# Optimization experiments

Hardware: AMD Instinct MI355X
Metric: run time of the kernel (lower is better)

## Reference

```python
import jax, jax.numpy as jnp
import numpy as np

T1 = 0.2
T2 = 1.2
LABEL_SMOOTHING = 0.05
NUM_ITERS = 20  # fixed-point iterations for lambda_t_a (t2 > 1 branch)


def log_t(x, t):
    # tempered log (t != 1)
    return (x ** (1.0 - t) - 1.0) / (1.0 - t)


def exp_t(x, t):
    # tempered exp (t != 1): relu((1-t)x + 1) ** (1/(1-t))
    return jnp.maximum((1.0 - t) * x + 1.0, 0.0) ** (1.0 / (1.0 - t))


def lambda_t_a(a, t):
    # t > 1 fixed-point branch of the original torch code, with a fixed
    # iteration count instead of a host-synced convergence check.
    mu = jnp.max(a, axis=-1, keepdims=True)            # [N, 1]
    norm_a_initial = a - mu                            # [N, C], <= 0

    def body(norm_a, _):
        z_a = jnp.sum(exp_t(norm_a, t), axis=-1, keepdims=True)  # [N, 1]
        return z_a ** (1.0 - t) * norm_a_initial, None

    norm_a, _ = jax.lax.scan(body, norm_a_initial, None, length=NUM_ITERS)
    z_a = jnp.sum(exp_t(norm_a, t), axis=-1, keepdims=True)
    return -log_t(1.0 / z_a, t) + mu                   # [N, 1]


def setup_inputs() -> dict:
    key = jax.random.key(0)
    k1, k2 = jax.random.split(key)
    N, C = 16384, 1000
    inputs = jax.random.normal(k1, (N, C), dtype=jnp.float32)
    labels = jax.random.randint(k2, (N,), 0, C)
    targets = jax.nn.one_hot(labels, C, dtype=jnp.float32)
    return {"inputs": inputs, "targets": targets}


def reference(inputs, targets):
    num_classes = targets.shape[-1]
    # label smoothing (label_smoothing > 0 branch)
    targets = (1.0 - num_classes / (num_classes - 1) * LABEL_SMOOTHING) * targets \
              + LABEL_SMOOTHING / (num_classes - 1)
    norm_constants = lambda_t_a(inputs, T2)                      # [N, 1]
    probabilities = exp_t(inputs - norm_constants, T2)           # [N, C]
    loss1 = targets * (log_t(targets + 1e-8, T1) - log_t(probabilities, T1))
    loss2 = (targets ** (2.0 - T1) - probabilities ** (2.0 - T1)) / (2.0 - T1)
    out = jnp.sum(loss1 - loss2, axis=-1)                        # [N]
    return jnp.mean(out)
```

## Files before the change

kernel.cpp:

```cpp
#include <hip/hip_runtime.h>
#include <math.h>

#define C_DIM 1000
#define BIG   1.0e30f

__device__ __forceinline__ float fexp2(float x) { return __builtin_amdgcn_exp2f(x); }
__device__ __forceinline__ float flog2(float x) { return __builtin_amdgcn_logf(x); }
__device__ __forceinline__ float frcp(float x)  { return __builtin_amdgcn_rcpf(x); }

template <int CTRL, int RM>
__device__ __forceinline__ float dpp_add_term(float x) {
    int y = __builtin_amdgcn_update_dpp(0, __float_as_int(x), CTRL, RM, 0xf, true);
    return __int_as_float(y);
}
template <int CTRL, int RM>
__device__ __forceinline__ float dpp_max_term(float x) {
    int y = __builtin_amdgcn_update_dpp(__float_as_int(x), __float_as_int(x), CTRL, RM, 0xf, false);
    return __int_as_float(y);
}

#define DPP_SUM_CHAIN(x)                      \
    x += dpp_add_term<0x111, 0xf>(x);         \
    x += dpp_add_term<0x112, 0xf>(x);         \
    x += dpp_add_term<0x114, 0xf>(x);         \
    x += dpp_add_term<0x118, 0xf>(x);         \
    x += dpp_add_term<0x142, 0xa>(x);         \
    x += dpp_add_term<0x143, 0xc>(x);

__device__ __forceinline__ float bcast63(float x) {
    return __int_as_float(__builtin_amdgcn_readlane(__float_as_int(x), 63));
}

__device__ __forceinline__ float wave_sum(float x) {
    DPP_SUM_CHAIN(x)
    return bcast63(x);
}

__device__ __forceinline__ float wave_max(float x) {
    x = fmaxf(x, dpp_max_term<0x111, 0xf>(x));
    x = fmaxf(x, dpp_max_term<0x112, 0xf>(x));
    x = fmaxf(x, dpp_max_term<0x114, 0xf>(x));
    x = fmaxf(x, dpp_max_term<0x118, 0xf>(x));
    x = fmaxf(x, dpp_max_term<0x142, 0xa>(x));
    x = fmaxf(x, dpp_max_term<0x143, 0xc>(x));
    return bcast63(x);
}

__global__ __launch_bounds__(256) void btll(
    const float* __restrict__ inputs, const float* __restrict__ targets,
    float* __restrict__ row_out, int n_rows,
    float C0, float E_off, float dE)
{
    const int lane = threadIdx.x & 63;
    const int wave = threadIdx.x >> 6;
    const int row  = blockIdx.x * 4 + wave;
    if (row >= n_rows) return;

    const float4* in4 = (const float4*)(inputs  + (size_t)row * C_DIM);
    const float4* tg4 = (const float4*)(targets + (size_t)row * C_DIM);
    const bool m3 = (lane + 192) < 250;

    float4 x0 = in4[lane];
    float4 x1 = in4[lane + 64];
    float4 x2 = in4[lane + 128];
    float4 x3 = m3 ? in4[lane + 192] : make_float4(-BIG, -BIG, -BIG, -BIG);
    float4 t0 = tg4[lane];
    float4 t1 = tg4[lane + 64];
    float4 t2 = tg4[lane + 128];
    float4 t3 = m3 ? tg4[lane + 192] : make_float4(0.f, 0.f, 0.f, 0.f);

    float a[16];
    a[0]=x0.x; a[1]=x0.y; a[2]=x0.z; a[3]=x0.w;
    a[4]=x1.x; a[5]=x1.y; a[6]=x1.z; a[7]=x1.w;
    a[8]=x2.x; a[9]=x2.y; a[10]=x2.z; a[11]=x2.w;
    a[12]=x3.x; a[13]=x3.y; a[14]=x3.z; a[15]=x3.w;

    float ah = 0.0f;
    ah = fmaf(t0.x, a[0], ah);  ah = fmaf(t0.y, a[1], ah);
    ah = fmaf(t0.z, a[2], ah);  ah = fmaf(t0.w, a[3], ah);
    ah = fmaf(t1.x, a[4], ah);  ah = fmaf(t1.y, a[5], ah);
    ah = fmaf(t1.z, a[6], ah);  ah = fmaf(t1.w, a[7], ah);
    ah = fmaf(t2.x, a[8], ah);  ah = fmaf(t2.y, a[9], ah);
    ah = fmaf(t2.z, a[10], ah); ah = fmaf(t2.w, a[11], ah);
    ah = fmaf(t3.x, a[12], ah); ah = fmaf(t3.y, a[13], ah);
    ah = fmaf(t3.z, a[14], ah); ah = fmaf(t3.w, a[15], ah);

    float mu = a[0];
    #pragma unroll
    for (int k = 1; k < 16; ++k) mu = fmaxf(mu, a[k]);
    mu = wave_max(mu);
    ah = wave_sum(ah);

    float b[16];
    #pragma unroll
    for (int k = 0; k < 16; ++k) b[k] = -0.2f * (a[k] - mu);
    const float hb = -0.2f * (ah - mu);

    float s = 0.0f;
    #pragma unroll
    for (int k = 0; k < 16; ++k) {
        float u = 1.0f + b[k];
        float u2 = u * u;
        s += frcp(u2 * u2 * u);
    }
    s = wave_sum(s);
    const float lam = fexp2(-0.2f * flog2(s));

    s = 0.0f;
    #pragma unroll
    for (int k = 0; k < 16; ++k) {
        float u = fmaf(lam, b[k], 1.0f);
        float u2 = u * u;
        s += frcp(u2 * u2 * u);
    }
    s = wave_sum(s);
    const float w = fexp2(0.2f * flog2(s));

    float S4 = 0.0f, S5 = 0.0f, S6 = 0.0f, S9 = 0.0f, S10 = 0.0f, S11 = 0.0f;
    #pragma unroll
    for (int k = 0; k < 16; ++k) {
        float r  = frcp(w + b[k]);
        float r2 = r * r;
        float r4 = r2 * r2;
        float r5 = r4 * r;
        float r9 = r4 * r5;
        S4  += r4;
        S5  += r5;
        S6  += r5 * r;
        S9  += r9;
        S10 += r5 * r5;
        S11 += r9 * r2;
    }
    DPP_SUM_CHAIN(S4)
    DPP_SUM_CHAIN(S5)
    DPP_SUM_CHAIN(S6)
    DPP_SUM_CHAIN(S9)
    DPP_SUM_CHAIN(S10)
    DPP_SUM_CHAIN(S11)
    S4 = bcast63(S4);  S5 = bcast63(S5);  S6 = bcast63(S6);
    S9 = bcast63(S9);  S10 = bcast63(S10); S11 = bcast63(S11);

    const float d   = (S5 - 1.0f) * 0.2f * frcp(S6);
    const float w1  = w + d;
    const float d2  = d * d;
    const float S4c = S4 + fmaf(10.0f * d2, S6,  -4.0f * d * S5);
    const float S9c = S9 + fmaf(45.0f * d2, S11, -9.0f * d * S10);
    const float rh  = frcp(w1 + hb);
    const float rh2 = rh * rh;
    const float rh4 = rh2 * rh2;

    const float loss = fmaf(-E_off, S4c,
                       fmaf(-dE, rh4,
                       fmaf(1.0f / 1.8f, S9c, C0)));
    if (lane == 0) row_out[row] = loss;
}

__global__ __launch_bounds__(1024) void reduce_mean(
    const float* __restrict__ row_out, float* __restrict__ out, int n)
{
    __shared__ double sm[16];
    const int lane = threadIdx.x & 63;
    const int wv   = threadIdx.x >> 6;
    double s = 0.0;
    for (int i = threadIdx.x; i < n; i += 1024) s += (double)row_out[i];
    #pragma unroll
    for (int off = 32; off > 0; off >>= 1) s += __shfl_xor(s, off, 64);
    if (lane == 0) sm[wv] = s;
    __syncthreads();
    if (wv == 0) {
        double t = (lane < 16) ? sm[lane] : 0.0;
        #pragma unroll
        for (int off = 32; off > 0; off >>= 1) t += __shfl_xor(t, off, 64);
        if (lane == 0) out[0] = (float)(t / (double)n);
    }
}

extern "C" void kernel_launch(void* const* d_in, const int* in_sizes, int n_in,
                              void* d_out, int out_size, void* d_ws, size_t ws_size,
                              hipStream_t stream) {
    const float* inputs  = (const float*)d_in[0];
    const float* targets = (const float*)d_in[1];
    float* out = (float*)d_out;

    const int N = in_sizes[0] / C_DIM;
    float* row_out = (float*)d_ws;

    const double ls    = 0.05;
    const double c1g_d = 1.0 - (1000.0 / 999.0) * ls;
    const double c2_d  = ls / 999.0;
    const float  tp_on_f  = (float)c1g_d + (float)c2_d;
    const float  tp_off_f = (float)c2_d;
    const double tp_on  = (double)tp_on_f;
    const double tp_off = (double)tp_off_f;
    const double A_on  = (pow(tp_on  + 1e-8, 0.8) - 1.0) / 0.8;
    const double A_off = (pow(tp_off + 1e-8, 0.8) - 1.0) / 0.8;
    const double B_on  = pow(tp_on,  1.8);
    const double B_off = pow(tp_off, 1.8);
    const double E_on_d  = 1.25 * tp_on;
    const double E_off_d = 1.25 * tp_off;
    const double F_on_d  = tp_on  * A_on  + E_on_d  - B_on  / 1.8;
    const double F_off_d = tp_off * A_off + E_off_d - B_off / 1.8;
    const double C0_d    = (C_DIM - 1) * F_off_d + F_on_d;
    const double dE_d    = E_on_d - E_off_d;

    dim3 grid((N + 3) / 4);
    btll<<<grid, 256, 0, stream>>>(inputs, targets, row_out, N,
                                   (float)C0_d, (float)E_off_d, (float)dE_d);
    reduce_mean<<<1, 1024, 0, stream>>>(row_out, out, N);
}
```

Before: 146.6 us.

## Process two rows per wave with early loads and algebraic shift folding

Each wave now handles two rows. All loads for both rows are issued up front so the second row's memory latency overlaps the first row's compute. The max-shift is folded into per-loop constants (bb = -0.2*x, offsets c1/c2/c3), which removes the per-element subtraction of mu, and launch bounds now request 8 blocks per SM. The final mean reduction uses float4 loads. This raises register pressure, which may limit occupancy, and halves the number of waves launched.

```diff
diff --git a/kernel.cpp b/kernel.cpp
--- a/kernel.cpp
+++ b/kernel.cpp
@@ -46,80 +46,73 @@
     return bcast63(x);
 }
 
-__global__ __launch_bounds__(256) void btll(
-    const float* __restrict__ inputs, const float* __restrict__ targets,
-    float* __restrict__ row_out, int n_rows,
-    float C0, float E_off, float dE)
-{
-    const int lane = threadIdx.x & 63;
-    const int wave = threadIdx.x >> 6;
-    const int row  = blockIdx.x * 4 + wave;
-    if (row >= n_rows) return;
-
-    const float4* in4 = (const float4*)(inputs  + (size_t)row * C_DIM);
-    const float4* tg4 = (const float4*)(targets + (size_t)row * C_DIM);
-    const bool m3 = (lane + 192) < 250;
-
-    float4 x0 = in4[lane];
-    float4 x1 = in4[lane + 64];
-    float4 x2 = in4[lane + 128];
-    float4 x3 = m3 ? in4[lane + 192] : make_float4(-BIG, -BIG, -BIG, -BIG);
-    float4 t0 = tg4[lane];
-    float4 t1 = tg4[lane + 64];
-    float4 t2 = tg4[lane + 128];
-    float4 t3 = m3 ? tg4[lane + 192] : make_float4(0.f, 0.f, 0.f, 0.f);
-
-    float a[16];
-    a[0]=x0.x; a[1]=x0.y; a[2]=x0.z; a[3]=x0.w;
-    a[4]=x1.x; a[5]=x1.y; a[6]=x1.z; a[7]=x1.w;
-    a[8]=x2.x; a[9]=x2.y; a[10]=x2.z; a[11]=x2.w;
-    a[12]=x3.x; a[13]=x3.y; a[14]=x3.z; a[15]=x3.w;
-
-    float ah = 0.0f;
-    ah = fmaf(t0.x, a[0], ah);  ah = fmaf(t0.y, a[1], ah);
-    ah = fmaf(t0.z, a[2], ah);  ah = fmaf(t0.w, a[3], ah);
-    ah = fmaf(t1.x, a[4], ah);  ah = fmaf(t1.y, a[5], ah);
-    ah = fmaf(t1.z, a[6], ah);  ah = fmaf(t1.w, a[7], ah);
-    ah = fmaf(t2.x, a[8], ah);  ah = fmaf(t2.y, a[9], ah);
-    ah = fmaf(t2.z, a[10], ah); ah = fmaf(t2.w, a[11], ah);
-    ah = fmaf(t3.x, a[12], ah); ah = fmaf(t3.y, a[13], ah);
-    ah = fmaf(t3.z, a[14], ah); ah = fmaf(t3.w, a[15], ah);
-
-    float mu = a[0];
-    #pragma unroll
-    for (int k = 1; k < 16; ++k) mu = fmaxf(mu, a[k]);
-    mu = wave_max(mu);
-    ah = wave_sum(ah);
-
-    float b[16];
-    #pragma unroll
-    for (int k = 0; k < 16; ++k) b[k] = -0.2f * (a[k] - mu);
-    const float hb = -0.2f * (ah - mu);
-
+__device__ __forceinline__ float tr16(const float4 x0, const float4 x1,
+                                      const float4 x2, const float4 x3,
+                                      float bb[16])
+{
+    bb[0]=-0.2f*x0.x;  bb[1]=-0.2f*x0.y;  bb[2]=-0.2f*x0.z;  bb[3]=-0.2f*x0.w;
+    bb[4]=-0.2f*x1.x;  bb[5]=-0.2f*x1.y;  bb[6]=-0.2f*x1.z;  bb[7]=-0.2f*x1.w;
+    bb[8]=-0.2f*x2.x;  bb[9]=-0.2f*x2.y;  bb[10]=-0.2f*x2.z; bb[11]=-0.2f*x2.w;
+    bb[12]=-0.2f*x3.x; bb[13]=-0.2f*x3.y; bb[14]=-0.2f*x3.z; bb[15]=-0.2f*x3.w;
+    float m0 = fmaxf(fmaxf(x0.x, x0.y), fmaxf(x0.z, x0.w));
+    float m1 = fmaxf(fmaxf(x1.x, x1.y), fmaxf(x1.z, x1.w));
+    float m2 = fmaxf(fmaxf(x2.x, x2.y), fmaxf(x2.z, x2.w));
+    float m3 = fmaxf(fmaxf(x3.x, x3.y), fmaxf(x3.z, x3.w));
+    return fmaxf(fmaxf(m0, m1), fmaxf(m2, m3));
+}
+
+__device__ __forceinline__ float dot16(const float4 t0, const float4 t1,
+                                       const float4 t2, const float4 t3,
+                                       const float bb[16])
+{
     float s = 0.0f;
+    s = fmaf(t0.x, bb[0],  s); s = fmaf(t0.y, bb[1],  s);
+    s = fmaf(t0.z, bb[2],  s); s = fmaf(t0.w, bb[3],  s);
+    s = fmaf(t1.x, bb[4],  s); s = fmaf(t1.y, bb[5],  s);
+    s = fmaf(t1.z, bb[6],  s); s = fmaf(t1.w, bb[7],  s);
+    s = fmaf(t2.x, bb[8],  s); s = fmaf(t2.y, bb[9],  s);
+    s = fmaf(t2.z, bb[10], s); s = fmaf(t2.w, bb[11], s);
+    s = fmaf(t3.x, bb[12], s); s = fmaf(t3.y, bb[13], s);
+    s = fmaf(t3.z, bb[14], s); s = fmaf(t3.w, bb[15], s);
+    return s;
+}
+
+__device__ __forceinline__ void row_core(const float bb[16], float mxl, float ahbl,
+                                         float* __restrict__ row_out, int row, int lane,
+                                         float C0, float E_off, float dE)
+{
+    const float mu  = wave_max(mxl);
+    const float ahb = wave_sum(ahbl);
+    const float g   = 0.2f * mu;
+    const float hb  = ahb + g;
+
+    const float c1 = 1.0f + g;
+    float s = 0.0f;
     #pragma unroll
     for (int k = 0; k < 16; ++k) {
-        float u = 1.0f + b[k];
+        float u = bb[k] + c1;
         float u2 = u * u;
         s += frcp(u2 * u2 * u);
     }
     s = wave_sum(s);
     const float lam = fexp2(-0.2f * flog2(s));
 
+    const float c2 = fmaf(lam, g, 1.0f);
     s = 0.0f;
     #pragma unroll
     for (int k = 0; k < 16; ++k) {
-        float u = fmaf(lam, b[k], 1.0f);
+        float u = fmaf(lam, bb[k], c2);
         float u2 = u * u;
         s += frcp(u2 * u2 * u);
     }
     s = wave_sum(s);
     const float w = fexp2(0.2f * flog2(s));
 
+    const float c3 = w + g;
     float S4 = 0.0f, S5 = 0.0f, S6 = 0.0f, S9 = 0.0f, S10 = 0.0f, S11 = 0.0f;
     #pragma unroll
     for (int k = 0; k < 16; ++k) {
-        float r  = frcp(w + b[k]);
+        float r  = frcp(bb[k] + c3);
         float r2 = r * r;
         float r4 = r2 * r2;
         float r5 = r4 * r;
@@ -155,14 +148,73 @@
     if (lane == 0) row_out[row] = loss;
 }
 
+__global__ __launch_bounds__(256, 8) void btll(
+    const float* __restrict__ inputs, const float* __restrict__ targets,
+    float* __restrict__ row_out, int n_rows,
+    float C0, float E_off, float dE)
+{
+    const int lane = threadIdx.x & 63;
+    const int wave = threadIdx.x >> 6;
+    const int wid  = blockIdx.x * 4 + wave;
+    int row0 = wid * 2;
+    if (row0 >= n_rows) return;
+    int row1 = row0 + 1;
+    const bool has1 = row1 < n_rows;
+    if (!has1) row1 = row0;
+
+    const float4* in0 = (const float4*)(inputs  + (size_t)row0 * C_DIM);
+    const float4* tg0 = (const float4*)(targets + (size_t)row0 * C_DIM);
+    const float4* in1 = (const float4*)(inputs  + (size_t)row1 * C_DIM);
+    const float4* tg1 = (const float4*)(targets + (size_t)row1 * C_DIM);
+    const bool m3 = (lane + 192) < 250;
+    const float4 xpad = make_float4(-BIG, -BIG, -BIG, -BIG);
+    const float4 tpad = make_float4(0.f, 0.f, 0.f, 0.f);
+
+    float4 a0 = in0[lane];
+    float4 a1 = in0[lane + 64];
+    float4 a2 = in0[lane + 128];
+    float4 a3 = m3 ? in0[lane + 192] : xpad;
+    float4 t0 = tg0[lane];
+    float4 t1 = tg0[lane + 64];
+    float4 t2 = tg0[lane + 128];
+    float4 t3 = m3 ? tg0[lane + 192] : tpad;
+    float4 p0 = in1[lane];
+    float4 p1 = in1[lane + 64];
+    float4 p2 = in1[lane + 128];
+    float4 p3 = m3 ? in1[lane + 192] : xpad;
+
+    float bbA[16];
+    float mxA = tr16(a0, a1, a2, a3, bbA);
+    float ahA = dot16(t0, t1, t2, t3, bbA);
+
+    float4 q0 = tg1[lane];
+    float4 q1 = tg1[lane + 64];
+    float4 q2 = tg1[lane + 128];
+    float4 q3 = m3 ? tg1[lane + 192] : tpad;
+
+    float bbB[16];
+    float mxB = tr16(p0, p1, p2, p3, bbB);
+    float ahB = dot16(q0, q1, q2, q3, bbB);
+
+    row_core(bbA, mxA, ahA, row_out, row0, lane, C0, E_off, dE);
+    if (has1) row_core(bbB, mxB, ahB, row_out, row1, lane, C0, E_off, dE);
+}
+
 __global__ __launch_bounds__(1024) void reduce_mean(
     const float* __restrict__ row_out, float* __restrict__ out, int n)
 {
     __shared__ double sm[16];
     const int lane = threadIdx.x & 63;
     const int wv   = threadIdx.x >> 6;
+    const int n4   = n >> 2;
+    const float4* r4 = (const float4*)row_out;
     double s = 0.0;
-    for (int i = threadIdx.x; i < n; i += 1024) s += (double)row_out[i];
+    for (int i = threadIdx.x; i < n4; i += 1024) {
+        float4 v = r4[i];
+        s += (double)v.x + (double)v.y + (double)v.z + (double)v.w;
+    }
+    if (threadIdx.x == 0)
+        for (int i = n4 << 2; i < n; ++i) s += (double)row_out[i];
     #pragma unroll
     for (int off = 32; off > 0; off >>= 1) s += __shfl_xor(s, off, 64);
     if (lane == 0) sm[wv] = s;
@@ -203,7 +255,7 @@
     const double C0_d    = (C_DIM - 1) * F_off_d + F_on_d;
     const double dE_d    = E_on_d - E_off_d;
 
-    dim3 grid((N + 3) / 4);
+    dim3 grid((N + 7) / 8);
     btll<<<grid, 256, 0, stream>>>(inputs, targets, row_out, N,
                                    (float)C0_d, (float)E_off_d, (float)dE_d);
     reduce_mean<<<1, 1024, 0, stream>>>(row_out, out, N);
```

New measurement: 168.6 us. 15.0% more time.
